# Performance work log

Measured on AMD Instinct MI355X. Metric: run time of the kernel, lower is better.

The kernel has to match this reference:

```python
import jax, jax.numpy as jnp
import numpy as np

B, L, C = 2, 2048, 2048
H, HKV, D = 16, 4, 128  # heads, kv heads, head_dim
G = H // HKV            # GQA group size
NEG = -1e9


def rms_norm(x, w, eps=1e-6):
    # FastRMSNorm: compute in fp32, scale by weight, cast back
    xf = x.astype(jnp.float32)
    y = xf * jax.lax.rsqrt(jnp.mean(xf * xf, axis=-1, keepdims=True) + eps) * w
    return y.astype(x.dtype)


def apply_rope(t, cos, sin):
    # t: (B, h, L, D); cos/sin: (L, D//2) broadcast to (1,1,L,D//2)
    t1, t2 = jnp.split(t, 2, axis=-1)
    c = cos[None, None]
    s = sin[None, None]
    return jnp.concatenate([t1 * c - t2 * s, t2 * c + t1 * s], axis=-1)


def setup_inputs() -> dict:
    key = jax.random.key(0)
    ks = jax.random.split(key, 8)
    x = jax.random.normal(ks[0], (B, L, C), jnp.float32)
    Wq = jax.random.normal(ks[1], (H * D, C), jnp.float32) * 0.02
    Wk = jax.random.normal(ks[2], (HKV * D, C), jnp.float32) * 0.02
    Wv = jax.random.normal(ks[3], (HKV * D, C), jnp.float32) * 0.02
    Wo = jax.random.normal(ks[4], (C, H * D), jnp.float32) * 0.02
    q_norm_w = jnp.ones((D,), jnp.float32)
    k_norm_w = jnp.ones((D,), jnp.float32)
    pos = jnp.arange(L, dtype=jnp.float32)[:, None]
    inv_freq = 1.0 / (10000.0 ** (jnp.arange(0, D, 2, dtype=jnp.float32) / D))
    ang = pos * inv_freq[None, :]            # (L, D//2)
    rope_cos = jnp.cos(ang)
    rope_sin = jnp.sin(ang)
    # VAR-style block-causal visibility: 8 blocks of 256, query block i sees key blocks <= i
    blk = jnp.arange(L) // 256
    vis = blk[None, :] <= blk[:, None]       # (L, L) bool
    attn_bias = jnp.where(vis, 0.0, NEG).astype(jnp.float32)[None, None]  # (1,1,L,L)
    return dict(x=x, Wq=Wq, Wk=Wk, Wv=Wv, Wo=Wo, q_norm_w=q_norm_w,
                k_norm_w=k_norm_w, rope_cos=rope_cos, rope_sin=rope_sin,
                attn_bias=attn_bias)


def reference(x, Wq, Wk, Wv, Wo, q_norm_w, k_norm_w, rope_cos, rope_sin, attn_bias):
    b, l, c = x.shape
    # fused projections -> (B, h, L, D)
    q = rms_norm((x @ Wq.T).reshape(b, l, H, D), q_norm_w).transpose(0, 2, 1, 3)
    k = rms_norm((x @ Wk.T).reshape(b, l, HKV, D), k_norm_w).transpose(0, 2, 1, 3)
    v = (x @ Wv.T).reshape(b, l, HKV, D).transpose(0, 2, 1, 3)
    q = apply_rope(q, rope_cos, rope_sin)
    k = apply_rope(k, rope_cos, rope_sin)
    scale = D ** -0.5
    # GQA: group query heads over kv heads
    qg = q.reshape(b, HKV, G, l, D)
    scores = jnp.einsum('bkgqd,bkKd->bkgqK', qg, k) * scale
    scores = scores + attn_bias[:, :, None]  # broadcast (1,1,1,L,L)
    probs = jax.nn.softmax(scores, axis=-1)
    out = jnp.einsum('bkgqK,bkKd->bkgqd', probs, v)
    out = out.reshape(b, H, l, D).transpose(0, 2, 1, 3).reshape(b, l, H * D)
    return out @ Wo.T
```

## Files before the change

### kernel.cpp

```cpp
#include <hip/hip_runtime.h>

#define B_ 2
#define L_ 2048
#define C_ 2048
#define H_ 16
#define HKV_ 4
#define D_ 128
#define G_ (H_ / HKV_)
#define TOK_ (B_ * L_)
#define NQKV_ 3072

typedef __bf16 bf16;
typedef __bf16 bf16x4 __attribute__((ext_vector_type(4)));
typedef __bf16 bf16x8 __attribute__((ext_vector_type(8)));
typedef float f32x4 __attribute__((ext_vector_type(4)));

__device__ inline void gload16(const void* g, void* l) {
  __builtin_amdgcn_global_load_lds(
      (const __attribute__((address_space(1))) void*)g,
      (__attribute__((address_space(3))) void*)l, 16, 0, 0);
}

#define N4_X  2097152
#define N4_WQ 1048576
#define N4_WK 262144
#define N4_WV 262144
#define N4_WO 1048576
#define N4_TOT (N4_X + N4_WQ + N4_WK + N4_WV + N4_WO)

__global__ void cvt_all(const float* __restrict__ x, const float* __restrict__ wq,
                        const float* __restrict__ wk, const float* __restrict__ wv,
                        const float* __restrict__ wo, bf16* __restrict__ dst) {
  int stride = gridDim.x * blockDim.x;
  for (int j = blockIdx.x * blockDim.x + threadIdx.x; j < N4_TOT; j += stride) {
    const float* s;
    int off;
    if (j < N4_X) { s = x; off = j; }
    else if (j < N4_X + N4_WQ) { s = wq; off = j - N4_X; }
    else if (j < N4_X + N4_WQ + N4_WK) { s = wk; off = j - (N4_X + N4_WQ); }
    else if (j < N4_X + N4_WQ + N4_WK + N4_WV) { s = wv; off = j - (N4_X + N4_WQ + N4_WK); }
    else { s = wo; off = j - (N4_X + N4_WQ + N4_WK + N4_WV); }
    float4 v = reinterpret_cast<const float4*>(s)[off];
    bf16x4 o = {(bf16)v.x, (bf16)v.y, (bf16)v.z, (bf16)v.w};
    reinterpret_cast<bf16x4*>(dst)[j] = o;
  }
}

template <bool OUT_F32>
__global__ __launch_bounds__(256, 3) void gemm_bt(
    const bf16* __restrict__ A, const bf16* __restrict__ Bm,
    void* __restrict__ Cm, int M, int N, int K) {
  __shared__ __align__(16) bf16 sA[3][128 * 32];
  __shared__ __align__(16) bf16 sB[3][128 * 32];
  const int tid = threadIdx.x;
  const int row0 = blockIdx.x * 128, col0 = blockIdx.y * 128;
  const int wid = tid >> 6, lane = tid & 63;
  const int wr = wid >> 1, wc = wid & 1;
  const int l15 = lane & 15, kk = (lane >> 4) * 8;
  f32x4 acc[4][4] = {};
  const int nk = K / 32;
  const int r0 = tid >> 2, c0 = tid & 3;
  const int r1 = 64 + r0, c1 = c0;
  const int ldsA0 = (wid * 64) * 8, ldsA1 = (256 + wid * 64) * 8;

  auto stage = [&](int kt, int slot) {
    gload16(A + (size_t)(row0 + r0) * K + kt * 32 + c0 * 8, &sA[slot][ldsA0]);
    gload16(A + (size_t)(row0 + r1) * K + kt * 32 + c1 * 8, &sA[slot][ldsA1]);
    gload16(Bm + (size_t)(col0 + r0) * K + kt * 32 + c0 * 8, &sB[slot][ldsA0]);
    gload16(Bm + (size_t)(col0 + r1) * K + kt * 32 + c1 * 8, &sB[slot][ldsA1]);
  };

  stage(0, 0);
  stage(1, 1);
  asm volatile("s_waitcnt vmcnt(4)" ::: "memory");
  __builtin_amdgcn_s_barrier();
  __builtin_amdgcn_sched_barrier(0);

  int slot = 0;
  for (int kt = 0; kt < nk; ++kt) {
    int s2 = slot + 2; if (s2 >= 3) s2 -= 3;
    if (kt + 2 < nk) stage(kt + 2, s2);
    const bf16* cA = sA[slot];
    const bf16* cB = sB[slot];
    bf16x8 af[4], bfr[4];
#pragma unroll
    for (int m = 0; m < 4; ++m)
      af[m] = *reinterpret_cast<const bf16x8*>(cA + (wr * 64 + m * 16 + l15) * 32 + kk);
#pragma unroll
    for (int n = 0; n < 4; ++n)
      bfr[n] = *reinterpret_cast<const bf16x8*>(cB + (wc * 64 + n * 16 + l15) * 32 + kk);
    __builtin_amdgcn_s_setprio(1);
#pragma unroll
    for (int m = 0; m < 4; ++m)
#pragma unroll
      for (int n = 0; n < 4; ++n)
        acc[m][n] = __builtin_amdgcn_mfma_f32_16x16x32_bf16(af[m], bfr[n], acc[m][n], 0, 0, 0);
    __builtin_amdgcn_s_setprio(0);
    if (kt + 2 < nk)
      asm volatile("s_waitcnt vmcnt(4)" ::: "memory");
    else
      asm volatile("s_waitcnt vmcnt(0)" ::: "memory");
    __builtin_amdgcn_s_barrier();
    __builtin_amdgcn_sched_barrier(0);
    slot = (slot + 1 == 3) ? 0 : slot + 1;
  }
#pragma unroll
  for (int m = 0; m < 4; ++m)
#pragma unroll
    for (int n = 0; n < 4; ++n)
#pragma unroll
      for (int r = 0; r < 4; ++r) {
        int row = row0 + wr * 64 + m * 16 + (lane >> 4) * 4 + r;
        int col = col0 + wc * 64 + n * 16 + l15;
        if constexpr (OUT_F32)
          reinterpret_cast<float*>(Cm)[(size_t)row * N + col] = acc[m][n][r];
        else
          reinterpret_cast<bf16*>(Cm)[(size_t)row * N + col] = (bf16)acc[m][n][r];
      }
}

__global__ void k_norm_rope(const bf16* __restrict__ proj,
                            const float* __restrict__ normw,
                            const float* __restrict__ cosb,
                            const float* __restrict__ sinb,
                            bf16* __restrict__ out) {
  int wid = (blockIdx.x * blockDim.x + threadIdx.x) >> 6;
  int lane = threadIdx.x & 63;
  int head = wid & 3, tok = wid >> 2;
  int b = tok / L_, l = tok % L_;
  const bf16* p = proj + (size_t)tok * NQKV_ + H_ * D_ + head * D_;
  float t1 = (float)p[lane];
  float t2 = (float)p[lane + 64];
  float ss = t1 * t1 + t2 * t2;
#pragma unroll
  for (int off = 32; off; off >>= 1) ss += __shfl_xor(ss, off);
  float r = rsqrtf(ss * (1.0f / 128.0f) + 1e-6f);
  float n1 = t1 * r * normw[lane];
  float n2 = t2 * r * normw[lane + 64];
  float c = cosb[l * 64 + lane], s = sinb[l * 64 + lane];
  bf16* q = out + (((size_t)b * HKV_ + head) * L_ + l) * D_;
  q[lane] = (bf16)(n1 * c - n2 * s);
  q[lane + 64] = (bf16)(n2 * c + n1 * s);
}

__global__ __launch_bounds__(256) void v_transpose(const bf16* __restrict__ proj,
                                                   bf16* __restrict__ vt) {
  __shared__ __align__(16) bf16 sT[64 * 136];
  const int t = threadIdx.x;
  const int l0 = blockIdx.x * 64;
  const int bk = blockIdx.y;
  const bf16* src = proj + (size_t)((bk >> 2) * L_ + l0) * NQKV_ + (H_ + HKV_) * D_ + (bk & 3) * D_;
#pragma unroll
  for (int c = 0; c < 4; ++c) {
    int idx = c * 256 + t;
    int l = idx >> 4, dc = idx & 15;
    bf16x8 v = *reinterpret_cast<const bf16x8*>(src + (size_t)l * NQKV_ + dc * 8);
    *reinterpret_cast<bf16x8*>((char*)sT + l * 272 + ((dc ^ (l >> 3)) << 4)) = v;
  }
  __syncthreads();
  bf16* dst = vt + (size_t)bk * D_ * L_ + l0;
#pragma unroll
  for (int c = 0; c < 4; ++c) {
    int idx = c * 256 + t;
    int d = idx >> 3, lg = idx & 7;
    bf16x8 o;
#pragma unroll
    for (int j = 0; j < 8; ++j) {
      int l = lg * 8 + j;
      o[j] = *reinterpret_cast<const bf16*>((char*)sT + l * 272 + (((d >> 3) ^ lg) << 4) + (d & 7) * 2);
    }
    *reinterpret_cast<bf16x8*>(dst + (size_t)d * L_ + lg * 8) = o;
  }
}

#define SM_K0 0
#define SM_K1 16384
#define SM_V0 32768
#define SM_V1 49152
#define SM_P  65536
__global__ __launch_bounds__(512, 4) void attn_fused(
    const bf16* __restrict__ QKV,
    const bf16* __restrict__ Kn,
    const bf16* __restrict__ Vt,
    const float* __restrict__ qnw,
    const float* __restrict__ cosb, const float* __restrict__ sinb,
    bf16* __restrict__ AO) {
  __shared__ __align__(16) char smem[81920];
  const int tid = threadIdx.x;
  const int wid = tid >> 6, lane = tid & 63;
  const int bid = blockIdx.x;
  const int bk = bid & 7;
  const int qt = (bid < 256) ? (bid >> 3) : 63 - ((bid - 256) >> 3);
  const int b = bk >> 2;
  const int hl = wid & 3, qs = wid >> 2;
  const int h = (bk & 3) * G_ + hl;
  const int qrow0 = qt * 32 + qs * 16;
  const int l15 = lane & 15, g4 = lane >> 4, kk = g4 * 8;
  const int swz = (l15 & 7) << 4;

  const int qrow = qrow0 + l15;
  const bf16* qsrc = QKV + (size_t)(b * L_ + qrow) * NQKV_ + h * D_;
  float t[4][8];
  float ss = 0.f;
#pragma unroll
  for (int c = 0; c < 4; ++c) {
    bf16x8 v = *reinterpret_cast<const bf16x8*>(qsrc + c * 32 + kk);
#pragma unroll
    for (int j = 0; j < 8; ++j) { t[c][j] = (float)v[j]; ss += t[c][j] * t[c][j]; }
  }

  const int kr0 = tid >> 4, kc0 = tid & 15;
  const int kr1 = 32 + kr0;
  const int vr0 = tid >> 3, vc0 = tid & 7;
  const int vr1 = 64 + vr0;
  const bf16* kb = Kn + (size_t)bk * L_ * D_;
  const bf16* vb = Vt + (size_t)bk * D_ * (size_t)L_;
  const bf16* kp0 = kb + (size_t)kr0 * D_ + ((kc0 ^ (kr0 & 7)) * 8);
  const bf16* kp1 = kb + (size_t)kr1 * D_ + ((kc0 ^ (kr1 & 7)) * 8);
  const bf16* vp0 = vb + (size_t)vr0 * L_ + ((vc0 ^ (vr0 & 7)) * 8);
  const bf16* vp1 = vb + (size_t)vr1 * L_ + ((vc0 ^ (vr1 & 7)) * 8);

  const int ntiles = ((qt >> 3) + 1) * 4;
  gload16(kp0, smem + SM_K0 + tid * 16);
  gload16(kp1, smem + SM_K0 + 8192 + tid * 16);
  gload16(vp0, smem + SM_V0 + tid * 16);
  gload16(vp1, smem + SM_V0 + 8192 + tid * 16);

  constexpr float SCL = 0.12752650038632816f;
  ss += __shfl_xor(ss, 16);
  ss += __shfl_xor(ss, 32);
  const float rr = rsqrtf(ss * (1.0f / 128.0f) + 1e-6f);
  bf16x8 qf[4];
#pragma unroll
  for (int c = 0; c < 2; ++c)
#pragma unroll
    for (int j = 0; j < 8; ++j) {
      int i = c * 32 + kk + j;
      float n1 = t[c][j] * rr * qnw[i];
      float n2 = t[c + 2][j] * rr * qnw[i + 64];
      float cs = cosb[qrow * 64 + i], sn = sinb[qrow * 64 + i];
      qf[c][j] = (bf16)((n1 * cs - n2 * sn) * SCL);
      qf[c + 2][j] = (bf16)((n2 * cs + n1 * sn) * SCL);
    }

  int aK[4], aV[2], aPw[4];
#pragma unroll
  for (int c = 0; c < 4; ++c)
    aK[c] = l15 * 256 + ((((c << 2) + g4) ^ (l15 & 7)) << 4);
#pragma unroll
  for (int hh = 0; hh < 2; ++hh)
    aV[hh] = l15 * 128 + ((((hh << 2) + g4) ^ (l15 & 7)) << 4);
  const int pbase = SM_P + wid * 2048 + l15 * 128;
#pragma unroll
  for (int n = 0; n < 4; ++n)
    aPw[n] = pbase + (((n << 5) + (g4 << 3)) ^ swz);
  const int aPr0 = pbase + ((g4 << 4) ^ swz);
  const int aPr1 = pbase + ((64 + (g4 << 4)) ^ swz);

  f32x4 acc[8] = {};
  float mref = -1e30f, lpart = 0.f;

  __syncthreads();

  auto tile_step = [&](int KB, int VB, int KBn, int VBn, int ktNext, bool doPref) {
    if (doPref) {
      gload16(kp0 + (size_t)ktNext * 64 * D_, smem + KBn + tid * 16);
      gload16(kp1 + (size_t)ktNext * 64 * D_, smem + KBn + 8192 + tid * 16);
      gload16(vp0 + ktNext * 64, smem + VBn + tid * 16);
      gload16(vp1 + ktNext * 64, smem + VBn + 8192 + tid * 16);
    }
    f32x4 s[4];
    __builtin_amdgcn_s_setprio(1);
#pragma unroll
    for (int n = 0; n < 4; ++n) {
      f32x4 st = {};
#pragma unroll
      for (int c = 0; c < 4; ++c) {
        bf16x8 kf = *reinterpret_cast<const bf16x8*>(smem + KB + n * 4096 + aK[c]);
        st = __builtin_amdgcn_mfma_f32_16x16x32_bf16(kf, qf[c], st, 0, 0, 0);
      }
      s[n] = st;
    }
    __builtin_amdgcn_s_setprio(0);
    float pm = fmaxf(fmaxf(s[0][0], s[0][1]), fmaxf(s[0][2], s[0][3]));
#pragma unroll
    for (int n = 1; n < 4; ++n)
      pm = fmaxf(pm, fmaxf(fmaxf(s[n][0], s[n][1]), fmaxf(s[n][2], s[n][3])));
    if (!__all(pm <= mref + 8.f)) {
      pm = fmaxf(pm, __shfl_xor(pm, 16));
      pm = fmaxf(pm, __shfl_xor(pm, 32));
      float mnew = fmaxf(mref, pm);
      float resc = exp2f(mref - mnew);
      mref = mnew;
      lpart *= resc;
#pragma unroll
      for (int f = 0; f < 8; ++f) acc[f] *= resc;
    }
#pragma unroll
    for (int n = 0; n < 4; ++n)
#pragma unroll
      for (int r = 0; r < 4; ++r) {
        float p = exp2f(s[n][r] - mref);
        s[n][r] = p;
        lpart += p;
      }
#pragma unroll
    for (int n = 0; n < 4; ++n) {
      bf16x4 pw = {(bf16)s[n][0], (bf16)s[n][1], (bf16)s[n][2], (bf16)s[n][3]};
      *reinterpret_cast<bf16x4*>(smem + aPw[n]) = pw;
    }
    bf16x8 pf0 = *reinterpret_cast<const bf16x8*>(smem + aPr0);
    bf16x8 pf1 = *reinterpret_cast<const bf16x8*>(smem + aPr1);
    __builtin_amdgcn_s_setprio(1);
#pragma unroll
    for (int f = 0; f < 8; ++f) {
      bf16x8 vf0 = *reinterpret_cast<const bf16x8*>(smem + VB + f * 2048 + aV[0]);
      acc[f] = __builtin_amdgcn_mfma_f32_16x16x32_bf16(vf0, pf0, acc[f], 0, 0, 0);
      bf16x8 vf1 = *reinterpret_cast<const bf16x8*>(smem + VB + f * 2048 + aV[1]);
      acc[f] = __builtin_amdgcn_mfma_f32_16x16x32_bf16(vf1, pf1, acc[f], 0, 0, 0);
    }
    __builtin_amdgcn_s_setprio(0);
    __syncthreads();
  };

  for (int kt = 0; kt < ntiles; kt += 2) {
    tile_step(SM_K0, SM_V0, SM_K1, SM_V1, kt + 1, true);
    tile_step(SM_K1, SM_V1, SM_K0, SM_V0, kt + 2, kt + 2 < ntiles);
  }

  lpart += __shfl_xor(lpart, 16);
  lpart += __shfl_xor(lpart, 32);
  const float rinv = 1.f / lpart;
  bf16* aop = AO + ((size_t)(b * L_ + qrow0 + l15) * H_ + h) * D_ + (g4 << 2);
#pragma unroll
  for (int f = 0; f < 8; ++f) {
    bf16x4 o = {(bf16)(acc[f][0] * rinv), (bf16)(acc[f][1] * rinv),
                (bf16)(acc[f][2] * rinv), (bf16)(acc[f][3] * rinv)};
    *reinterpret_cast<bf16x4*>(aop + f * 16) = o;
  }
}

extern "C" void kernel_launch(void* const* d_in, const int* in_sizes, int n_in,
                              void* d_out, int out_size, void* d_ws, size_t ws_size,
                              hipStream_t stream) {
  const float* x = (const float*)d_in[0];
  const float* Wq = (const float*)d_in[1];
  const float* Wk = (const float*)d_in[2];
  const float* Wv = (const float*)d_in[3];
  const float* Wo = (const float*)d_in[4];
  const float* qnw = (const float*)d_in[5];
  const float* knw = (const float*)d_in[6];
  const float* rc = (const float*)d_in[7];
  const float* rs = (const float*)d_in[8];
  float* out = (float*)d_out;

  char* ws = (char*)d_ws;
  bf16* xb = (bf16*)ws;    ws += (size_t)TOK_ * C_ * 2;
  bf16* wqb = (bf16*)ws;   ws += (size_t)(H_ * D_) * C_ * 2;
  bf16* wkb = (bf16*)ws;   ws += (size_t)(HKV_ * D_) * C_ * 2;
  bf16* wvb = (bf16*)ws;   ws += (size_t)(HKV_ * D_) * C_ * 2;
  bf16* wob = (bf16*)ws;   ws += (size_t)C_ * (H_ * D_) * 2;
  bf16* qkv = (bf16*)ws;   ws += (size_t)TOK_ * NQKV_ * 2;
  bf16* Kb = (bf16*)ws;    ws += (size_t)TOK_ * HKV_ * D_ * 2;
  bf16* Vtb = (bf16*)ws;   ws += (size_t)TOK_ * HKV_ * D_ * 2;
  bf16* AOb = xb;

  cvt_all<<<2048, 256, 0, stream>>>(x, Wq, Wk, Wv, Wo, xb);

  gemm_bt<false><<<dim3(TOK_ / 128, NQKV_ / 128), 256, 0, stream>>>(
      xb, wqb, qkv, TOK_, NQKV_, C_);

  k_norm_rope<<<(TOK_ * HKV_) / 4, 256, 0, stream>>>(qkv, knw, rc, rs, Kb);
  v_transpose<<<dim3(L_ / 64, B_ * HKV_), 256, 0, stream>>>(qkv, Vtb);

  attn_fused<<<512, 512, 0, stream>>>(qkv, Kb, Vtb, qnw, rc, rs, AOb);

  gemm_bt<true><<<dim3(TOK_ / 128, C_ / 128), 256, 0, stream>>>(
      AOb, wob, out, TOK_, C_, H_ * D_);
}
```

Before: 201.0 us.

## Give each attention wave two 16-row query groups to reuse K/V fragments

The attention kernel drops from 8 waves to 4 waves per block. Each wave now handles one head across both 16-row query groups, so every K and V fragment read from LDS feeds two MFMAs instead of one. This halves LDS fragment traffic per MFMA and raises the work done per wave. In exchange register pressure roughly doubles (two accumulator sets and two query fragment sets), fewer waves are available to hide latency, and each thread issues more global-to-LDS loads per tile.

```diff
diff --git a/kernel.cpp b/kernel.cpp
--- a/kernel.cpp
+++ b/kernel.cpp
@@ -178,7 +178,7 @@
 #define SM_V0 32768
 #define SM_V1 49152
 #define SM_P  65536
-__global__ __launch_bounds__(512, 4) void attn_fused(
+__global__ __launch_bounds__(256, 2) void attn_fused(
     const bf16* __restrict__ QKV,
     const bf16* __restrict__ Kn,
     const bf16* __restrict__ Vt,
@@ -192,56 +192,54 @@
   const int bk = bid & 7;
   const int qt = (bid < 256) ? (bid >> 3) : 63 - ((bid - 256) >> 3);
   const int b = bk >> 2;
-  const int hl = wid & 3, qs = wid >> 2;
-  const int h = (bk & 3) * G_ + hl;
-  const int qrow0 = qt * 32 + qs * 16;
+  const int h = (bk & 3) * G_ + wid;
+  const int qrow0 = qt * 32;
   const int l15 = lane & 15, g4 = lane >> 4, kk = g4 * 8;
   const int swz = (l15 & 7) << 4;
 
-  const int qrow = qrow0 + l15;
-  const bf16* qsrc = QKV + (size_t)(b * L_ + qrow) * NQKV_ + h * D_;
-  float t[4][8];
-  float ss = 0.f;
-#pragma unroll
-  for (int c = 0; c < 4; ++c) {
-    bf16x8 v = *reinterpret_cast<const bf16x8*>(qsrc + c * 32 + kk);
-#pragma unroll
-    for (int j = 0; j < 8; ++j) { t[c][j] = (float)v[j]; ss += t[c][j] * t[c][j]; }
-  }
-
   const int kr0 = tid >> 4, kc0 = tid & 15;
-  const int kr1 = 32 + kr0;
   const int vr0 = tid >> 3, vc0 = tid & 7;
-  const int vr1 = 64 + vr0;
   const bf16* kb = Kn + (size_t)bk * L_ * D_;
   const bf16* vb = Vt + (size_t)bk * D_ * (size_t)L_;
   const bf16* kp0 = kb + (size_t)kr0 * D_ + ((kc0 ^ (kr0 & 7)) * 8);
-  const bf16* kp1 = kb + (size_t)kr1 * D_ + ((kc0 ^ (kr1 & 7)) * 8);
   const bf16* vp0 = vb + (size_t)vr0 * L_ + ((vc0 ^ (vr0 & 7)) * 8);
-  const bf16* vp1 = vb + (size_t)vr1 * L_ + ((vc0 ^ (vr1 & 7)) * 8);
 
   const int ntiles = ((qt >> 3) + 1) * 4;
-  gload16(kp0, smem + SM_K0 + tid * 16);
-  gload16(kp1, smem + SM_K0 + 8192 + tid * 16);
-  gload16(vp0, smem + SM_V0 + tid * 16);
-  gload16(vp1, smem + SM_V0 + 8192 + tid * 16);
+#pragma unroll
+  for (int j = 0; j < 4; ++j) {
+    gload16(kp0 + (size_t)(16 * j) * D_, smem + SM_K0 + j * 4096 + tid * 16);
+    gload16(vp0 + (size_t)(32 * j) * L_, smem + SM_V0 + j * 4096 + tid * 16);
+  }
 
   constexpr float SCL = 0.12752650038632816f;
-  ss += __shfl_xor(ss, 16);
-  ss += __shfl_xor(ss, 32);
-  const float rr = rsqrtf(ss * (1.0f / 128.0f) + 1e-6f);
-  bf16x8 qf[4];
-#pragma unroll
-  for (int c = 0; c < 2; ++c)
-#pragma unroll
-    for (int j = 0; j < 8; ++j) {
-      int i = c * 32 + kk + j;
-      float n1 = t[c][j] * rr * qnw[i];
-      float n2 = t[c + 2][j] * rr * qnw[i + 64];
-      float cs = cosb[qrow * 64 + i], sn = sinb[qrow * 64 + i];
-      qf[c][j] = (bf16)((n1 * cs - n2 * sn) * SCL);
-      qf[c + 2][j] = (bf16)((n2 * cs + n1 * sn) * SCL);
-    }
+  bf16x8 qf[2][4];
+#pragma unroll
+  for (int qg = 0; qg < 2; ++qg) {
+    const int qrow = qrow0 + qg * 16 + l15;
+    const bf16* qs = QKV + (size_t)(b * L_ + qrow) * NQKV_ + h * D_;
+    float tt[4][8];
+    float ss = 0.f;
+#pragma unroll
+    for (int c = 0; c < 4; ++c) {
+      bf16x8 v = *reinterpret_cast<const bf16x8*>(qs + c * 32 + kk);
+#pragma unroll
+      for (int j = 0; j < 8; ++j) { tt[c][j] = (float)v[j]; ss += tt[c][j] * tt[c][j]; }
+    }
+    ss += __shfl_xor(ss, 16);
+    ss += __shfl_xor(ss, 32);
+    const float rr = rsqrtf(ss * (1.0f / 128.0f) + 1e-6f);
+#pragma unroll
+    for (int c = 0; c < 2; ++c)
+#pragma unroll
+      for (int j = 0; j < 8; ++j) {
+        int i = c * 32 + kk + j;
+        float n1 = tt[c][j] * rr * qnw[i];
+        float n2 = tt[c + 2][j] * rr * qnw[i + 64];
+        float cs = cosb[qrow * 64 + i], sn = sinb[qrow * 64 + i];
+        qf[qg][c][j] = (bf16)((n1 * cs - n2 * sn) * SCL);
+        qf[qg][c + 2][j] = (bf16)((n2 * cs + n1 * sn) * SCL);
+      }
+  }
 
   int aK[4], aV[2], aPw[4];
 #pragma unroll
@@ -250,74 +248,89 @@
 #pragma unroll
   for (int hh = 0; hh < 2; ++hh)
     aV[hh] = l15 * 128 + ((((hh << 2) + g4) ^ (l15 & 7)) << 4);
-  const int pbase = SM_P + wid * 2048 + l15 * 128;
-#pragma unroll
+  const int pbase = SM_P + wid * 4096 + l15 * 128;
+  #pragma unroll
   for (int n = 0; n < 4; ++n)
     aPw[n] = pbase + (((n << 5) + (g4 << 3)) ^ swz);
   const int aPr0 = pbase + ((g4 << 4) ^ swz);
   const int aPr1 = pbase + ((64 + (g4 << 4)) ^ swz);
 
-  f32x4 acc[8] = {};
-  float mref = -1e30f, lpart = 0.f;
+  f32x4 acc0[8] = {}, acc1[8] = {};
+  float mref0 = -1e30f, lpart0 = 0.f, mref1 = -1e30f, lpart1 = 0.f;
 
   __syncthreads();
 
   auto tile_step = [&](int KB, int VB, int KBn, int VBn, int ktNext, bool doPref) {
     if (doPref) {
-      gload16(kp0 + (size_t)ktNext * 64 * D_, smem + KBn + tid * 16);
-      gload16(kp1 + (size_t)ktNext * 64 * D_, smem + KBn + 8192 + tid * 16);
-      gload16(vp0 + ktNext * 64, smem + VBn + tid * 16);
-      gload16(vp1 + ktNext * 64, smem + VBn + 8192 + tid * 16);
-    }
-    f32x4 s[4];
+#pragma unroll
+      for (int j = 0; j < 4; ++j) {
+        gload16(kp0 + (size_t)(ktNext * 64 + 16 * j) * D_, smem + KBn + j * 4096 + tid * 16);
+        gload16(vp0 + (size_t)(32 * j) * L_ + ktNext * 64, smem + VBn + j * 4096 + tid * 16);
+      }
+    }
+    f32x4 s0[4], s1[4];
     __builtin_amdgcn_s_setprio(1);
 #pragma unroll
     for (int n = 0; n < 4; ++n) {
-      f32x4 st = {};
+      f32x4 t0 = {}, t1 = {};
 #pragma unroll
       for (int c = 0; c < 4; ++c) {
         bf16x8 kf = *reinterpret_cast<const bf16x8*>(smem + KB + n * 4096 + aK[c]);
-        st = __builtin_amdgcn_mfma_f32_16x16x32_bf16(kf, qf[c], st, 0, 0, 0);
-      }
-      s[n] = st;
+        t0 = __builtin_amdgcn_mfma_f32_16x16x32_bf16(kf, qf[0][c], t0, 0, 0, 0);
+        t1 = __builtin_amdgcn_mfma_f32_16x16x32_bf16(kf, qf[1][c], t1, 0, 0, 0);
+      }
+      s0[n] = t0;
+      s1[n] = t1;
     }
     __builtin_amdgcn_s_setprio(0);
-    float pm = fmaxf(fmaxf(s[0][0], s[0][1]), fmaxf(s[0][2], s[0][3]));
-#pragma unroll
-    for (int n = 1; n < 4; ++n)
-      pm = fmaxf(pm, fmaxf(fmaxf(s[n][0], s[n][1]), fmaxf(s[n][2], s[n][3])));
-    if (!__all(pm <= mref + 8.f)) {
-      pm = fmaxf(pm, __shfl_xor(pm, 16));
-      pm = fmaxf(pm, __shfl_xor(pm, 32));
-      float mnew = fmaxf(mref, pm);
-      float resc = exp2f(mref - mnew);
-      mref = mnew;
-      lpart *= resc;
-#pragma unroll
-      for (int f = 0; f < 8; ++f) acc[f] *= resc;
+    float pm0 = fmaxf(fmaxf(s0[0][0], s0[0][1]), fmaxf(s0[0][2], s0[0][3]));
+    float pm1 = fmaxf(fmaxf(s1[0][0], s1[0][1]), fmaxf(s1[0][2], s1[0][3]));
+#pragma unroll
+    for (int n = 1; n < 4; ++n) {
+      pm0 = fmaxf(pm0, fmaxf(fmaxf(s0[n][0], s0[n][1]), fmaxf(s0[n][2], s0[n][3])));
+      pm1 = fmaxf(pm1, fmaxf(fmaxf(s1[n][0], s1[n][1]), fmaxf(s1[n][2], s1[n][3])));
+    }
+    if (!__all((pm0 <= mref0 + 8.f) & (pm1 <= mref1 + 8.f))) {
+      pm0 = fmaxf(pm0, __shfl_xor(pm0, 16));
+      pm0 = fmaxf(pm0, __shfl_xor(pm0, 32));
+      pm1 = fmaxf(pm1, __shfl_xor(pm1, 16));
+      pm1 = fmaxf(pm1, __shfl_xor(pm1, 32));
+      float mn0 = fmaxf(mref0, pm0), mn1 = fmaxf(mref1, pm1);
+      float rs0 = exp2f(mref0 - mn0), rs1 = exp2f(mref1 - mn1);
+      mref0 = mn0; mref1 = mn1;
+      lpart0 *= rs0; lpart1 *= rs1;
+#pragma unroll
+      for (int f = 0; f < 8; ++f) { acc0[f] *= rs0; acc1[f] *= rs1; }
     }
 #pragma unroll
     for (int n = 0; n < 4; ++n)
 #pragma unroll
       for (int r = 0; r < 4; ++r) {
-        float p = exp2f(s[n][r] - mref);
-        s[n][r] = p;
-        lpart += p;
+        float p0 = exp2f(s0[n][r] - mref0);
+        float p1 = exp2f(s1[n][r] - mref1);
+        s0[n][r] = p0; s1[n][r] = p1;
+        lpart0 += p0; lpart1 += p1;
       }
 #pragma unroll
     for (int n = 0; n < 4; ++n) {
-      bf16x4 pw = {(bf16)s[n][0], (bf16)s[n][1], (bf16)s[n][2], (bf16)s[n][3]};
-      *reinterpret_cast<bf16x4*>(smem + aPw[n]) = pw;
-    }
-    bf16x8 pf0 = *reinterpret_cast<const bf16x8*>(smem + aPr0);
-    bf16x8 pf1 = *reinterpret_cast<const bf16x8*>(smem + aPr1);
+      bf16x4 w0 = {(bf16)s0[n][0], (bf16)s0[n][1], (bf16)s0[n][2], (bf16)s0[n][3]};
+      bf16x4 w1 = {(bf16)s1[n][0], (bf16)s1[n][1], (bf16)s1[n][2], (bf16)s1[n][3]};
+      *reinterpret_cast<bf16x4*>(smem + aPw[n]) = w0;
+      *reinterpret_cast<bf16x4*>(smem + aPw[n] + 2048) = w1;
+    }
+    bf16x8 pf00 = *reinterpret_cast<const bf16x8*>(smem + aPr0);
+    bf16x8 pf01 = *reinterpret_cast<const bf16x8*>(smem + aPr1);
+    bf16x8 pf10 = *reinterpret_cast<const bf16x8*>(smem + aPr0 + 2048);
+    bf16x8 pf11 = *reinterpret_cast<const bf16x8*>(smem + aPr1 + 2048);
     __builtin_amdgcn_s_setprio(1);
 #pragma unroll
     for (int f = 0; f < 8; ++f) {
       bf16x8 vf0 = *reinterpret_cast<const bf16x8*>(smem + VB + f * 2048 + aV[0]);
-      acc[f] = __builtin_amdgcn_mfma_f32_16x16x32_bf16(vf0, pf0, acc[f], 0, 0, 0);
       bf16x8 vf1 = *reinterpret_cast<const bf16x8*>(smem + VB + f * 2048 + aV[1]);
-      acc[f] = __builtin_amdgcn_mfma_f32_16x16x32_bf16(vf1, pf1, acc[f], 0, 0, 0);
+      acc0[f] = __builtin_amdgcn_mfma_f32_16x16x32_bf16(vf0, pf00, acc0[f], 0, 0, 0);
+      acc0[f] = __builtin_amdgcn_mfma_f32_16x16x32_bf16(vf1, pf01, acc0[f], 0, 0, 0);
+      acc1[f] = __builtin_amdgcn_mfma_f32_16x16x32_bf16(vf0, pf10, acc1[f], 0, 0, 0);
+      acc1[f] = __builtin_amdgcn_mfma_f32_16x16x32_bf16(vf1, pf11, acc1[f], 0, 0, 0);
     }
     __builtin_amdgcn_s_setprio(0);
     __syncthreads();
@@ -328,15 +341,21 @@
     tile_step(SM_K1, SM_V1, SM_K0, SM_V0, kt + 2, kt + 2 < ntiles);
   }
 
-  lpart += __shfl_xor(lpart, 16);
-  lpart += __shfl_xor(lpart, 32);
-  const float rinv = 1.f / lpart;
-  bf16* aop = AO + ((size_t)(b * L_ + qrow0 + l15) * H_ + h) * D_ + (g4 << 2);
+  lpart0 += __shfl_xor(lpart0, 16);
+  lpart0 += __shfl_xor(lpart0, 32);
+  lpart1 += __shfl_xor(lpart1, 16);
+  lpart1 += __shfl_xor(lpart1, 32);
+  const float ri0 = 1.f / lpart0, ri1 = 1.f / lpart1;
+  bf16* ap0 = AO + ((size_t)(b * L_ + qrow0 + l15) * H_ + h) * D_ + (g4 << 2);
+  bf16* ap1 = AO + ((size_t)(b * L_ + qrow0 + 16 + l15) * H_ + h) * D_ + (g4 << 2);
 #pragma unroll
   for (int f = 0; f < 8; ++f) {
-    bf16x4 o = {(bf16)(acc[f][0] * rinv), (bf16)(acc[f][1] * rinv),
-                (bf16)(acc[f][2] * rinv), (bf16)(acc[f][3] * rinv)};
-    *reinterpret_cast<bf16x4*>(aop + f * 16) = o;
+    bf16x4 o0 = {(bf16)(acc0[f][0] * ri0), (bf16)(acc0[f][1] * ri0),
+                 (bf16)(acc0[f][2] * ri0), (bf16)(acc0[f][3] * ri0)};
+    bf16x4 o1 = {(bf16)(acc1[f][0] * ri1), (bf16)(acc1[f][1] * ri1),
+                 (bf16)(acc1[f][2] * ri1), (bf16)(acc1[f][3] * ri1)};
+    *reinterpret_cast<bf16x4*>(ap0 + f * 16) = o0;
+    *reinterpret_cast<bf16x4*>(ap1 + f * 16) = o1;
   }
 }
 
@@ -373,7 +392,7 @@
   k_norm_rope<<<(TOK_ * HKV_) / 4, 256, 0, stream>>>(qkv, knw, rc, rs, Kb);
   v_transpose<<<dim3(L_ / 64, B_ * HKV_), 256, 0, stream>>>(qkv, Vtb);
 
-  attn_fused<<<512, 512, 0, stream>>>(qkv, Kb, Vtb, qnw, rc, rs, AOb);
+  attn_fused<<<512, 256, 0, stream>>>(qkv, Kb, Vtb, qnw, rc, rs, AOb);
 
   gemm_bt<true><<<dim3(TOK_ / 128, C_ / 128), 256, 0, stream>>>(
       AOb, wob, out, TOK_, C_, H_ * D_);
```

Result: slower. 205.2 us (+2.1%).
